# Kernel tuning notes

Hardware: AMD Instinct MI355X
Metric: run time of the kernel (lower is better)

The kernel has to match this reference:

```python
import jax, jax.numpy as jnp
import numpy as np

# GridEncoder(d=3, L=16, F=2, b=2, N_min=16, log2_hashmap_size=19, gridtype='hash'), bound=1
D = 3
L = 16
F = 2
N_MIN = 16
PLS = 2.0            # per_level_scale b
LOG2_T = 19
BOUND = 1.0
N_CORNERS = 2 ** D
# fast_hash primes from the CUDA kernel (first D entries)
PRIMES = (np.uint32(1), np.uint32(2654435761), np.uint32(805459861))


def _offsets_and_res():
    """Replicates the Python offsets loop and the kernel's per-level resolution."""
    S = np.log2(PLS)
    offs = [0]
    res = []
    off = 0
    for l in range(L):
        scale = np.exp2(l * S) * N_MIN - 1.0      # kernel: scale = exp2f(level*S)*H - 1
        res.append(int(np.ceil(scale)) + 1)       # kernel: resolution = ceil(scale)+1
        N_l = int(np.ceil(N_MIN * PLS ** l))
        T = min(2 ** LOG2_T, (N_l + 1) ** D)
        off += T
        offs.append(off)
    return offs, res

OFFSETS, RES = _offsets_and_res()  # OFFSETS[-1] == 7131219


def setup_inputs() -> dict:
    k1, k2 = jax.random.split(jax.random.key(0))
    inputs = jax.random.uniform(k1, (1_000_000, D), jnp.float32, -1.0, 1.0)
    embeddings = jax.random.uniform(k2, (OFFSETS[-1], F), jnp.float32, -1e-4, 1e-4)
    return {"inputs": inputs, "embeddings": embeddings}


def _encode(inputs, embeddings):
    # normalize to [0,1] as in GridEncoder.forward
    x = (inputs + BOUND) / (2 * BOUND)            # [B, D]
    B = x.shape[0]
    S = np.log2(PLS)
    outs = []
    for l in range(L):  # fixed small level count -> Python loop is fine
        hmap = OFFSETS[l + 1] - OFFSETS[l]
        emb = embeddings[OFFSETS[l]:OFFSETS[l + 1]]   # static slice [hmap, F]
        resolution = RES[l]
        scale = np.float32(np.exp2(l * S) * N_MIN - 1.0)
        pos = x * scale + 0.5
        pg = jnp.floor(pos)
        frac = pos - pg                               # [B, D] in [0,1)
        pg = pg.astype(jnp.uint32)
        use_hash = (resolution + 1) ** D > hmap       # static per level
        acc = jnp.zeros((B, F), x.dtype)
        for corner in range(N_CORNERS):               # 8 corners, multilinear interp
            w = jnp.ones((B,), x.dtype)
            idx = jnp.zeros((B,), jnp.uint32)
            stride = 1
            for d in range(D):
                bit = (corner >> d) & 1
                g = pg[:, d] + np.uint32(bit)         # corner grid coord (uint32)
                w = w * (frac[:, d] if bit else (1.0 - frac[:, d]))
                if use_hash:
                    idx = idx ^ (g * PRIMES[d])       # uint32 wraparound == fast_hash
                else:
                    idx = idx + g * np.uint32(stride)
                    stride *= (resolution + 1)
            idx = (idx % np.uint32(hmap)).astype(jnp.int32)
            acc = acc + w[:, None] * emb[idx]         # gather [B, F]
        outs.append(acc)
    return jnp.concatenate(outs, axis=-1)             # [B, L*F], level-major like permute+reshape


def reference(inputs, embeddings):
    return _encode(inputs, embeddings)
```

## Files before the change

kernel.cpp:

```cpp
#include <hip/hip_runtime.h>
#include <cstdint>


static constexpr uint32_t kOff[17] = {
    0u, 4913u, 40850u, 315475u, 839763u, 1364051u, 1888339u, 2412627u,
    2936915u, 3461203u, 3985491u, 4509779u, 5034067u, 5558355u, 6082643u,
    6606931u, 7131219u};

static constexpr uint32_t P1 = 2654435761u;
static constexpr uint32_t P2 = 805459861u;

typedef float f4a8 __attribute__((ext_vector_type(4), aligned(8)));

__device__ __forceinline__ float to_unit(float v) {
  return __fmul_rn(__fadd_rn(v, 1.0f), 0.5f);
}

template <int LV>
__device__ __forceinline__ void pos_decomp(float x0, float x1, float x2,
                                           uint32_t& i0, uint32_t& i1,
                                           uint32_t& i2, float& f0, float& f1,
                                           float& f2) {
  constexpr float scale = (float)(16u << LV) - 1.0f;
  float p0 = __fadd_rn(__fmul_rn(x0, scale), 0.5f);
  float p1 = __fadd_rn(__fmul_rn(x1, scale), 0.5f);
  float p2 = __fadd_rn(__fmul_rn(x2, scale), 0.5f);
  float g0 = floorf(p0), g1 = floorf(p1), g2 = floorf(p2);
  f0 = __fsub_rn(p0, g0);
  f1 = __fsub_rn(p1, g1);
  f2 = __fsub_rn(p2, g2);
  i0 = (uint32_t)g0;
  i1 = (uint32_t)g1;
  i2 = (uint32_t)g2;
}

template <int LV>
__device__ __forceinline__ void hashed_accum(float x0, float x1, float x2,
                                             const float* __restrict__ embf,
                                             float& A0, float& A1) {
  static_assert(LV >= 3, "");
  constexpr uint32_t off = kOff[LV];
  constexpr uint32_t mask = 0x7FFFFu;
  uint32_t i0, i1, i2;
  float f0, f1, f2;
  pos_decomp<LV>(x0, x1, x2, i0, i1, i2, f0, f1, f2);

  const float w0l = __fsub_rn(1.0f, f0), w0h = f0;
  const float w1v[2] = {__fsub_rn(1.0f, f1), f1};
  const float w2v[2] = {__fsub_rn(1.0f, f2), f2};
  uint32_t h1v[2], h2v[2];
  h1v[0] = i1 * P1;
  h1v[1] = h1v[0] + P1;
  h2v[0] = i2 * P2;
  h2v[1] = h2v[0] + P2;

  const float2* t2 = (const float2*)embf + off;
  const bool odd = (i0 & 1u) != 0u;

  float acc0 = A0, acc1 = A1;
#pragma unroll
  for (int b2 = 0; b2 < 2; ++b2) {
#pragma unroll
    for (int b1 = 0; b1 < 2; ++b1) {
      const uint32_t ex = h1v[b1] ^ h2v[b2];
      const uint32_t ilo = (i0 ^ ex) & mask;
      const f4a8 v = *(const f4a8*)(t2 + (ilo & ~1u));
      const bool hs = (ilo & 1u) != 0u;
      float eL0 = hs ? v.z : v.x;
      float eL1 = hs ? v.w : v.y;
      float eH0 = hs ? v.x : v.z;
      float eH1 = hs ? v.y : v.w;
      if (odd) {
        const uint32_t ihi = ((i0 + 1u) ^ ex) & mask;
        const float2 e = t2[ihi];
        eH0 = e.x;
        eH1 = e.y;
      }
      const float wl = __fmul_rn(__fmul_rn(w0l, w1v[b1]), w2v[b2]);
      const float wh = __fmul_rn(__fmul_rn(w0h, w1v[b1]), w2v[b2]);
      acc0 = __fadd_rn(acc0, __fmul_rn(wl, eL0));
      acc1 = __fadd_rn(acc1, __fmul_rn(wl, eL1));
      acc0 = __fadd_rn(acc0, __fmul_rn(wh, eH0));
      acc1 = __fadd_rn(acc1, __fmul_rn(wh, eH1));
    }
  }
  A0 = acc0;
  A1 = acc1;
}

template <int LV>
__device__ __forceinline__ void dense_accum(float x0, float x1, float x2,
                                            const float* __restrict__ embf,
                                            float& A0, float& A1) {
  static_assert(LV < 3, "");
  constexpr uint32_t res = 16u << LV;
  constexpr uint32_t off = kOff[LV];
  constexpr uint32_t s1 = res + 1u, s2 = s1 * s1;
  uint32_t i0, i1, i2;
  float f0, f1, f2;
  pos_decomp<LV>(x0, x1, x2, i0, i1, i2, f0, f1, f2);

  const float w0l = __fsub_rn(1.0f, f0), w0h = f0;
  const float w1v[2] = {__fsub_rn(1.0f, f1), f1};
  const float w2v[2] = {__fsub_rn(1.0f, f2), f2};
  const uint32_t base = i0 + i1 * s1 + i2 * s2;
  const float2* t2 = (const float2*)embf + off;

  float acc0 = A0, acc1 = A1;
#pragma unroll
  for (int b2 = 0; b2 < 2; ++b2) {
#pragma unroll
    for (int b1 = 0; b1 < 2; ++b1) {
      const uint32_t idx = base + (b1 ? s1 : 0u) + (b2 ? s2 : 0u);
      const f4a8 v = *(const f4a8*)(t2 + idx);
      const float wl = __fmul_rn(__fmul_rn(w0l, w1v[b1]), w2v[b2]);
      const float wh = __fmul_rn(__fmul_rn(w0h, w1v[b1]), w2v[b2]);
      acc0 = __fadd_rn(acc0, __fmul_rn(wl, v.x));
      acc1 = __fadd_rn(acc1, __fmul_rn(wl, v.y));
      acc0 = __fadd_rn(acc0, __fmul_rn(wh, v.z));
      acc1 = __fadd_rn(acc1, __fmul_rn(wh, v.w));
    }
  }
  A0 = acc0;
  A1 = acc1;
}

template <int LV>
__device__ __forceinline__ void any_accum(float x0, float x1, float x2,
                                          const float* __restrict__ embf,
                                          float& A0, float& A1) {
  if constexpr (LV < 3)
    dense_accum<LV>(x0, x1, x2, embf, A0, A1);
  else
    hashed_accum<LV>(x0, x1, x2, embf, A0, A1);
}


template <int LV>
__global__ __launch_bounds__(256) void level_kernel(
    const float* __restrict__ in, const float* __restrict__ embf,
    float2* __restrict__ ws, int B) {
  const int q = blockIdx.x * 256 + threadIdx.x;
  const int p0 = q << 1;
  if (p0 >= B) return;
  const int p1 = p0 + 1;
  const float2* in2 = (const float2*)in;
  const size_t b3 = (size_t)q * 3;
  const float2 u0 = in2[b3], u1 = in2[b3 + 1], u2 = in2[b3 + 2];

  float a0 = 0.0f, a1 = 0.0f;
  hashed_accum<LV>(to_unit(u0.x), to_unit(u0.y), to_unit(u1.x), embf, a0, a1);

  float2* __restrict__ wsl = ws + (size_t)(LV - 3) * B;
  if (((B & 1) == 0) && p1 < B) {
    float b0 = 0.0f, b1f = 0.0f;
    hashed_accum<LV>(to_unit(u1.y), to_unit(u2.x), to_unit(u2.y), embf, b0,
                     b1f);
    *reinterpret_cast<float4*>(wsl + p0) = make_float4(a0, a1, b0, b1f);
  } else {
    wsl[p0] = make_float2(a0, a1);
    if (p1 < B) {
      float b0 = 0.0f, b1f = 0.0f;
      hashed_accum<LV>(to_unit(u1.y), to_unit(u2.x), to_unit(u2.y), embf, b0,
                       b1f);
      wsl[p1] = make_float2(b0, b1f);
    }
  }
}


__global__ __launch_bounds__(256) void final_kernel(
    const float* __restrict__ in, const float* __restrict__ embf,
    const float2* __restrict__ ws, float4* __restrict__ out4, int B) {
  __shared__ float4 lds[8 * 257];
  const int tid = threadIdx.x;
  const int p = blockIdx.x * 256 + tid;

  float a[32];
#pragma unroll
  for (int i = 0; i < 32; ++i) a[i] = 0.0f;

  if (p < B) {
    const float x0 = to_unit(in[(size_t)p * 3 + 0]);
    const float x1 = to_unit(in[(size_t)p * 3 + 1]);
    const float x2 = to_unit(in[(size_t)p * 3 + 2]);
    dense_accum<0>(x0, x1, x2, embf, a[0], a[1]);
    dense_accum<1>(x0, x1, x2, embf, a[2], a[3]);
    dense_accum<2>(x0, x1, x2, embf, a[4], a[5]);
#pragma unroll
    for (int l = 3; l < 16; ++l) {
      const float2 e = ws[(size_t)(l - 3) * B + p];
      a[2 * l] = e.x;
      a[2 * l + 1] = e.y;
    }
  }

#pragma unroll
  for (int w = 0; w < 8; ++w)
    lds[w * 257 + tid] = make_float4(a[4 * w], a[4 * w + 1], a[4 * w + 2],
                                     a[4 * w + 3]);
  __syncthreads();

  const size_t gbase = (size_t)blockIdx.x * 2048;
  const size_t lim = (size_t)B * 8;
#pragma unroll
  for (int j = 0; j < 8; ++j) {
    const int gl = j * 256 + tid;
    const size_t g = gbase + gl;
    if (g < lim) out4[g] = lds[(gl & 7) * 257 + (gl >> 3)];
  }
}


template <int LBASE>
__global__ __launch_bounds__(256) void grid_enc_kernel(
    const float* __restrict__ in, const float* __restrict__ embf,
    float* __restrict__ out, int B) {
  const int p = blockIdx.x * 256 + threadIdx.x;
  if (p >= B) return;
  const float x0 = to_unit(in[(size_t)p * 3 + 0]);
  const float x1 = to_unit(in[(size_t)p * 3 + 1]);
  const float x2 = to_unit(in[(size_t)p * 3 + 2]);

  float a[16];
#pragma unroll
  for (int i = 0; i < 16; ++i) a[i] = 0.0f;

  any_accum<LBASE + 0>(x0, x1, x2, embf, a[0], a[1]);
  any_accum<LBASE + 1>(x0, x1, x2, embf, a[2], a[3]);
  any_accum<LBASE + 2>(x0, x1, x2, embf, a[4], a[5]);
  any_accum<LBASE + 3>(x0, x1, x2, embf, a[6], a[7]);
  any_accum<LBASE + 4>(x0, x1, x2, embf, a[8], a[9]);
  any_accum<LBASE + 5>(x0, x1, x2, embf, a[10], a[11]);
  any_accum<LBASE + 6>(x0, x1, x2, embf, a[12], a[13]);
  any_accum<LBASE + 7>(x0, x1, x2, embf, a[14], a[15]);

  float4* __restrict__ o = (float4*)(out + (size_t)p * 32 + LBASE * 2);
  o[0] = make_float4(a[0], a[1], a[2], a[3]);
  o[1] = make_float4(a[4], a[5], a[6], a[7]);
  o[2] = make_float4(a[8], a[9], a[10], a[11]);
  o[3] = make_float4(a[12], a[13], a[14], a[15]);
}

extern "C" void kernel_launch(void* const* d_in, const int* in_sizes, int n_in,
                              void* d_out, int out_size, void* d_ws,
                              size_t ws_size, hipStream_t stream) {
  const float* in = (const float*)d_in[0];
  const float* emb = (const float*)d_in[1];
  float* out = (float*)d_out;
  const int B = in_sizes[0] / 3;
  const int blocksP = (B + 255) / 256;
  const int blocksQ = ((B + 1) / 2 + 255) / 256;
  const size_t ws_needed = (size_t)13 * (size_t)B * sizeof(float2);

  if (ws_size >= ws_needed) {
    float2* ws = (float2*)d_ws;
    level_kernel<3><<<blocksQ, 256, 0, stream>>>(in, emb, ws, B);
    level_kernel<4><<<blocksQ, 256, 0, stream>>>(in, emb, ws, B);
    level_kernel<5><<<blocksQ, 256, 0, stream>>>(in, emb, ws, B);
    level_kernel<6><<<blocksQ, 256, 0, stream>>>(in, emb, ws, B);
    level_kernel<7><<<blocksQ, 256, 0, stream>>>(in, emb, ws, B);
    level_kernel<8><<<blocksQ, 256, 0, stream>>>(in, emb, ws, B);
    level_kernel<9><<<blocksQ, 256, 0, stream>>>(in, emb, ws, B);
    level_kernel<10><<<blocksQ, 256, 0, stream>>>(in, emb, ws, B);
    level_kernel<11><<<blocksQ, 256, 0, stream>>>(in, emb, ws, B);
    level_kernel<12><<<blocksQ, 256, 0, stream>>>(in, emb, ws, B);
    level_kernel<13><<<blocksQ, 256, 0, stream>>>(in, emb, ws, B);
    level_kernel<14><<<blocksQ, 256, 0, stream>>>(in, emb, ws, B);
    level_kernel<15><<<blocksQ, 256, 0, stream>>>(in, emb, ws, B);
    final_kernel<<<blocksP, 256, 0, stream>>>(in, emb, ws, (float4*)out, B);
  } else {
    grid_enc_kernel<0><<<blocksP, 256, 0, stream>>>(in, emb, out, B);
    grid_enc_kernel<8><<<blocksP, 256, 0, stream>>>(in, emb, out, B);
  }
}
```

Before: 678.2 us.

## Merge per-level kernels into one zoned mega-kernel plus a transpose pass

```diff
diff --git a/kernel.cpp b/kernel.cpp
--- a/kernel.cpp
+++ b/kernel.cpp
@@ -11,17 +11,37 @@
 static constexpr uint32_t P2 = 805459861u;
 
 typedef float f4a8 __attribute__((ext_vector_type(4), aligned(8)));
+typedef float v2f __attribute__((ext_vector_type(2)));
+typedef float v4f __attribute__((ext_vector_type(4)));
+
+__device__ __forceinline__ float2 ntload2(const float2* p) {
+  v2f t = __builtin_nontemporal_load((const v2f*)p);
+  return make_float2(t[0], t[1]);
+}
+__device__ __forceinline__ void ntstore2(float2* p, float a, float b) {
+  v2f t;
+  t[0] = a;
+  t[1] = b;
+  __builtin_nontemporal_store(t, (v2f*)p);
+}
+__device__ __forceinline__ void ntstore4(float4* p, float a, float b, float c,
+                                         float d) {
+  v4f t;
+  t[0] = a;
+  t[1] = b;
+  t[2] = c;
+  t[3] = d;
+  __builtin_nontemporal_store(t, (v4f*)p);
+}
 
 __device__ __forceinline__ float to_unit(float v) {
   return __fmul_rn(__fadd_rn(v, 1.0f), 0.5f);
 }
 
-template <int LV>
-__device__ __forceinline__ void pos_decomp(float x0, float x1, float x2,
-                                           uint32_t& i0, uint32_t& i1,
-                                           uint32_t& i2, float& f0, float& f1,
-                                           float& f2) {
-  constexpr float scale = (float)(16u << LV) - 1.0f;
+__device__ __forceinline__ void pos_decomp_rt(float x0, float x1, float x2,
+                                              float scale, uint32_t& i0,
+                                              uint32_t& i1, uint32_t& i2,
+                                              float& f0, float& f1, float& f2) {
   float p0 = __fadd_rn(__fmul_rn(x0, scale), 0.5f);
   float p1 = __fadd_rn(__fmul_rn(x1, scale), 0.5f);
   float p2 = __fadd_rn(__fmul_rn(x2, scale), 0.5f);
@@ -34,16 +54,14 @@
   i2 = (uint32_t)g2;
 }
 
-template <int LV>
-__device__ __forceinline__ void hashed_accum(float x0, float x1, float x2,
-                                             const float* __restrict__ embf,
-                                             float& A0, float& A1) {
-  static_assert(LV >= 3, "");
-  constexpr uint32_t off = kOff[LV];
+__device__ __forceinline__ void hashed_accum_rt(float x0, float x1, float x2,
+                                                float scale,
+                                                const float2* __restrict__ t2,
+                                                float& A0, float& A1) {
   constexpr uint32_t mask = 0x7FFFFu;
   uint32_t i0, i1, i2;
   float f0, f1, f2;
-  pos_decomp<LV>(x0, x1, x2, i0, i1, i2, f0, f1, f2);
+  pos_decomp_rt(x0, x1, x2, scale, i0, i1, i2, f0, f1, f2);
 
   const float w0l = __fsub_rn(1.0f, f0), w0h = f0;
   const float w1v[2] = {__fsub_rn(1.0f, f1), f1};
@@ -54,9 +72,7 @@
   h2v[0] = i2 * P2;
   h2v[1] = h2v[0] + P2;
 
-  const float2* t2 = (const float2*)embf + off;
   const bool odd = (i0 & 1u) != 0u;
-
   float acc0 = A0, acc1 = A1;
 #pragma unroll
   for (int b2 = 0; b2 < 2; ++b2) {
@@ -96,9 +112,10 @@
   constexpr uint32_t res = 16u << LV;
   constexpr uint32_t off = kOff[LV];
   constexpr uint32_t s1 = res + 1u, s2 = s1 * s1;
+  constexpr float scale = (float)res - 1.0f;
   uint32_t i0, i1, i2;
   float f0, f1, f2;
-  pos_decomp<LV>(x0, x1, x2, i0, i1, i2, f0, f1, f2);
+  pos_decomp_rt(x0, x1, x2, scale, i0, i1, i2, f0, f1, f2);
 
   const float w0l = __fsub_rn(1.0f, f0), w0h = f0;
   const float w1v[2] = {__fsub_rn(1.0f, f1), f1};
@@ -125,92 +142,105 @@
   A1 = acc1;
 }
 
+
+__global__ __launch_bounds__(256) void mega_kernel(
+    const float* __restrict__ in, const float* __restrict__ embf,
+    float2* __restrict__ ws, int B, int NB) {
+  const int zone = blockIdx.x / NB;
+  const int q = (blockIdx.x - zone * NB) * 256 + threadIdx.x;
+  const int p0 = q << 1;
+  if (p0 >= B) return;
+  const bool hasB = (p0 + 1) < B;
+
+  float xA0, xA1, xA2, xB0 = 0.f, xB1 = 0.f, xB2 = 0.f;
+  if (hasB) {
+    const float2* in2 = (const float2*)in;
+    const size_t b3 = (size_t)q * 3;
+    const float2 u0 = ntload2(in2 + b3);
+    const float2 u1 = ntload2(in2 + b3 + 1);
+    const float2 u2 = ntload2(in2 + b3 + 2);
+    xA0 = to_unit(u0.x);
+    xA1 = to_unit(u0.y);
+    xA2 = to_unit(u1.x);
+    xB0 = to_unit(u1.y);
+    xB1 = to_unit(u2.x);
+    xB2 = to_unit(u2.y);
+  } else {
+    xA0 = to_unit(in[(size_t)p0 * 3 + 0]);
+    xA1 = to_unit(in[(size_t)p0 * 3 + 1]);
+    xA2 = to_unit(in[(size_t)p0 * 3 + 2]);
+  }
+  const bool pair4 = hasB && ((B & 1) == 0);
+
+  if (zone == 0) {
+    float a0, a1, b0, b1;
+#define DO_DENSE(LV)                                              \
+  a0 = a1 = b0 = b1 = 0.0f;                                       \
+  dense_accum<LV>(xA0, xA1, xA2, embf, a0, a1);                   \
+  if (hasB) dense_accum<LV>(xB0, xB1, xB2, embf, b0, b1);         \
+  {                                                               \
+    float2* wsl = ws + (size_t)LV * B;                            \
+    if (pair4)                                                    \
+      ntstore4((float4*)(wsl + p0), a0, a1, b0, b1);              \
+    else {                                                        \
+      ntstore2(wsl + p0, a0, a1);                                 \
+      if (hasB) ntstore2(wsl + p0 + 1, b0, b1);                   \
+    }                                                             \
+  }
+    DO_DENSE(0)
+    DO_DENSE(1)
+    DO_DENSE(2)
+#undef DO_DENSE
+  } else {
+    const int level = zone + 2;
+    const float scale = (float)(int)((16u << level) - 1u);
+    const float2* t2 =
+        (const float2*)embf + (315475u + (uint32_t)(level - 3) * 524288u);
+    float2* wsl = ws + (size_t)level * B;
+
+    float a0 = 0.0f, a1 = 0.0f;
+    hashed_accum_rt(xA0, xA1, xA2, scale, t2, a0, a1);
+    if (pair4) {
+      float b0 = 0.0f, b1 = 0.0f;
+      hashed_accum_rt(xB0, xB1, xB2, scale, t2, b0, b1);
+      ntstore4((float4*)(wsl + p0), a0, a1, b0, b1);
+    } else {
+      ntstore2(wsl + p0, a0, a1);
+      if (hasB) {
+        float b0 = 0.0f, b1 = 0.0f;
+        hashed_accum_rt(xB0, xB1, xB2, scale, t2, b0, b1);
+        ntstore2(wsl + p0 + 1, b0, b1);
+      }
+    }
+  }
+}
+
+
+__global__ __launch_bounds__(256) void transpose_kernel(
+    const float2* __restrict__ ws, float4* __restrict__ out4, size_t n4,
+    int B) {
+  const size_t g = (size_t)blockIdx.x * 256 + threadIdx.x;
+  if (g >= n4) return;
+  const int p = (int)(g >> 3);
+  const int j = (int)(g & 7);
+  const float2 e0 = ntload2(ws + (size_t)(2 * j) * B + p);
+  const float2 e1 = ntload2(ws + (size_t)(2 * j + 1) * B + p);
+  ntstore4(out4 + g, e0.x, e0.y, e1.x, e1.y);
+}
+
+
 template <int LV>
 __device__ __forceinline__ void any_accum(float x0, float x1, float x2,
                                           const float* __restrict__ embf,
                                           float& A0, float& A1) {
-  if constexpr (LV < 3)
+  if constexpr (LV < 3) {
     dense_accum<LV>(x0, x1, x2, embf, A0, A1);
-  else
-    hashed_accum<LV>(x0, x1, x2, embf, A0, A1);
-}
-
-
-template <int LV>
-__global__ __launch_bounds__(256) void level_kernel(
-    const float* __restrict__ in, const float* __restrict__ embf,
-    float2* __restrict__ ws, int B) {
-  const int q = blockIdx.x * 256 + threadIdx.x;
-  const int p0 = q << 1;
-  if (p0 >= B) return;
-  const int p1 = p0 + 1;
-  const float2* in2 = (const float2*)in;
-  const size_t b3 = (size_t)q * 3;
-  const float2 u0 = in2[b3], u1 = in2[b3 + 1], u2 = in2[b3 + 2];
-
-  float a0 = 0.0f, a1 = 0.0f;
-  hashed_accum<LV>(to_unit(u0.x), to_unit(u0.y), to_unit(u1.x), embf, a0, a1);
-
-  float2* __restrict__ wsl = ws + (size_t)(LV - 3) * B;
-  if (((B & 1) == 0) && p1 < B) {
-    float b0 = 0.0f, b1f = 0.0f;
-    hashed_accum<LV>(to_unit(u1.y), to_unit(u2.x), to_unit(u2.y), embf, b0,
-                     b1f);
-    *reinterpret_cast<float4*>(wsl + p0) = make_float4(a0, a1, b0, b1f);
-  } else {
-    wsl[p0] = make_float2(a0, a1);
-    if (p1 < B) {
-      float b0 = 0.0f, b1f = 0.0f;
-      hashed_accum<LV>(to_unit(u1.y), to_unit(u2.x), to_unit(u2.y), embf, b0,
-                       b1f);
-      wsl[p1] = make_float2(b0, b1f);
-    }
-  }
-}
-
-
-__global__ __launch_bounds__(256) void final_kernel(
-    const float* __restrict__ in, const float* __restrict__ embf,
-    const float2* __restrict__ ws, float4* __restrict__ out4, int B) {
-  __shared__ float4 lds[8 * 257];
-  const int tid = threadIdx.x;
-  const int p = blockIdx.x * 256 + tid;
-
-  float a[32];
-#pragma unroll
-  for (int i = 0; i < 32; ++i) a[i] = 0.0f;
-
-  if (p < B) {
-    const float x0 = to_unit(in[(size_t)p * 3 + 0]);
-    const float x1 = to_unit(in[(size_t)p * 3 + 1]);
-    const float x2 = to_unit(in[(size_t)p * 3 + 2]);
-    dense_accum<0>(x0, x1, x2, embf, a[0], a[1]);
-    dense_accum<1>(x0, x1, x2, embf, a[2], a[3]);
-    dense_accum<2>(x0, x1, x2, embf, a[4], a[5]);
-#pragma unroll
-    for (int l = 3; l < 16; ++l) {
-      const float2 e = ws[(size_t)(l - 3) * B + p];
-      a[2 * l] = e.x;
-      a[2 * l + 1] = e.y;
-    }
-  }
-
-#pragma unroll
-  for (int w = 0; w < 8; ++w)
-    lds[w * 257 + tid] = make_float4(a[4 * w], a[4 * w + 1], a[4 * w + 2],
-                                     a[4 * w + 3]);
-  __syncthreads();
-
-  const size_t gbase = (size_t)blockIdx.x * 2048;
-  const size_t lim = (size_t)B * 8;
-#pragma unroll
-  for (int j = 0; j < 8; ++j) {
-    const int gl = j * 256 + tid;
-    const size_t g = gbase + gl;
-    if (g < lim) out4[g] = lds[(gl & 7) * 257 + (gl >> 3)];
-  }
-}
-
+  } else {
+    constexpr float scale = (float)(16u << LV) - 1.0f;
+    const float2* t2 = (const float2*)embf + kOff[LV];
+    hashed_accum_rt(x0, x1, x2, scale, t2, A0, A1);
+  }
+}
 
 template <int LBASE>
 __global__ __launch_bounds__(256) void grid_enc_kernel(
@@ -249,27 +279,17 @@
   const float* emb = (const float*)d_in[1];
   float* out = (float*)d_out;
   const int B = in_sizes[0] / 3;
-  const int blocksP = (B + 255) / 256;
-  const int blocksQ = ((B + 1) / 2 + 255) / 256;
-  const size_t ws_needed = (size_t)13 * (size_t)B * sizeof(float2);
+  const size_t ws_needed = (size_t)16 * (size_t)B * sizeof(float2);
 
   if (ws_size >= ws_needed) {
     float2* ws = (float2*)d_ws;
-    level_kernel<3><<<blocksQ, 256, 0, stream>>>(in, emb, ws, B);
-    level_kernel<4><<<blocksQ, 256, 0, stream>>>(in, emb, ws, B);
-    level_kernel<5><<<blocksQ, 256, 0, stream>>>(in, emb, ws, B);
-    level_kernel<6><<<blocksQ, 256, 0, stream>>>(in, emb, ws, B);
-    level_kernel<7><<<blocksQ, 256, 0, stream>>>(in, emb, ws, B);
-    level_kernel<8><<<blocksQ, 256, 0, stream>>>(in, emb, ws, B);
-    level_kernel<9><<<blocksQ, 256, 0, stream>>>(in, emb, ws, B);
-    level_kernel<10><<<blocksQ, 256, 0, stream>>>(in, emb, ws, B);
-    level_kernel<11><<<blocksQ, 256, 0, stream>>>(in, emb, ws, B);
-    level_kernel<12><<<blocksQ, 256, 0, stream>>>(in, emb, ws, B);
-    level_kernel<13><<<blocksQ, 256, 0, stream>>>(in, emb, ws, B);
-    level_kernel<14><<<blocksQ, 256, 0, stream>>>(in, emb, ws, B);
-    level_kernel<15><<<blocksQ, 256, 0, stream>>>(in, emb, ws, B);
-    final_kernel<<<blocksP, 256, 0, stream>>>(in, emb, ws, (float4*)out, B);
-  } else {
+    const int NB = ((B + 1) / 2 + 255) / 256;
+    mega_kernel<<<NB * 14, 256, 0, stream>>>(in, emb, ws, B, NB);
+    const size_t n4 = (size_t)B * 8;
+    const int tb = (int)((n4 + 255) / 256);
+    transpose_kernel<<<tb, 256, 0, stream>>>(ws, (float4*)out, n4, B);
+  } else {
+    const int blocksP = (B + 255) / 256;
     grid_enc_kernel<0><<<blocksP, 256, 0, stream>>>(in, emb, out, B);
     grid_enc_kernel<8><<<blocksP, 256, 0, stream>>>(in, emb, out, B);
   }
```

New measurement: 708.0 us. 1.04x slower.
